# Kernel optimization log

Hardware: AMD Instinct MI355X
Metric: run time of the kernel (lower is better)

Reference implementation:

```python
import jax, jax.numpy as jnp
import numpy as np

B, T, C = 8, 2048, 1024  # batch, seq_len (== block_size), n_embed
HEAD = 64


def setup_inputs() -> dict:
    key = jax.random.key(0)
    k1, k2, k3, k4 = jax.random.split(key, 4)
    x = jax.random.normal(k1, (B, T, C), dtype=jnp.float32)
    # nn.Linear(n_embed, head_size, bias=False) -> weight [head, C]; stored as [C, head]
    Wk = jax.random.normal(k2, (C, HEAD), dtype=jnp.float32) * (C ** -0.5)
    Wq = jax.random.normal(k3, (C, HEAD), dtype=jnp.float32) * (C ** -0.5)
    Wv = jax.random.normal(k4, (C, HEAD), dtype=jnp.float32) * (C ** -0.5)
    return {"x": x, "Wk": Wk, "Wq": Wq, "Wv": Wv}


def reference(x, Wk, Wq, Wv):
    Bx, Tx, Cx = x.shape
    k = jnp.einsum('btc,ch->bth', x, Wk)  # [B,T,HEAD]
    q = jnp.einsum('btc,ch->bth', x, Wq)
    v = jnp.einsum('btc,ch->bth', x, Wv)
    # Source quirk: scores = k @ q^T (k rows), scaled by n_embed**-0.5 (C, not head_size)
    scores = jnp.einsum('bih,bjh->bij', k, q) * (Cx ** -0.5)  # [B,T,T]
    causal = jnp.tril(jnp.ones((Tx, Tx), dtype=bool))
    scores = jnp.where(causal, scores, -jnp.inf)
    attn = jax.nn.softmax(scores, axis=-1)
    out = jnp.einsum('bij,bjh->bih', attn, v)  # [B,T,HEAD]
    return out
```

## Files before the change

### kernel.cpp

```cpp
#include <hip/hip_runtime.h>
#include <cstdint>

#define B_ 8
#define T_ 2048
#define C_ 1024
#define H_ 64
#define BT_ (B_ * T_)

typedef short short8 __attribute__((ext_vector_type(8)));
typedef short bh4 __attribute__((ext_vector_type(4)));
typedef float f32x4 __attribute__((ext_vector_type(4)));

__device__ inline short f2bf(float f) {
  uint32_t u = __float_as_uint(f);
  u += 0x7fffu + ((u >> 16) & 1u);
  return (short)(u >> 16);
}

__device__ __forceinline__ void gl_lds16(const void* g, void* l) {
  __builtin_amdgcn_global_load_lds(
      (const __attribute__((address_space(1))) unsigned int*)g,
      (__attribute__((address_space(3))) unsigned int*)l, 16, 0, 0);
}

__global__ __launch_bounds__(256) void prep_w(
    const float* __restrict__ Wk, const float* __restrict__ Wq,
    const float* __restrict__ Wv, short* __restrict__ Wt) {
  __shared__ float wl[64][68];
  const int mat = blockIdx.x >> 4;
  const int kc = blockIdx.x & 15;
  const float* W = (mat == 0) ? Wk : (mat == 1) ? Wq : Wv;
  const float sc = (mat == 0) ? 0.03125f * 1.44269504088896f : 1.0f;
  const int t = threadIdx.x;
  const int k0 = kc * 64;
#pragma unroll
  for (int j = 0; j < 4; ++j) {
    int s = t + 256 * j;
    int kr = s >> 4, cf = s & 15;
    float4 v = *reinterpret_cast<const float4*>(&W[(size_t)(k0 + kr) * H_ + cf * 4]);
    wl[kr][cf * 4 + 0] = v.x; wl[kr][cf * 4 + 1] = v.y;
    wl[kr][cf * 4 + 2] = v.z; wl[kr][cf * 4 + 3] = v.w;
  }
  __syncthreads();
#pragma unroll
  for (int j = 0; j < 2; ++j) {
    int s = t + 256 * j;
    int n = s >> 3, g = s & 7;
    short8 o;
#pragma unroll
    for (int i = 0; i < 8; ++i) o[i] = f2bf(wl[8 * g + i][n] * sc);
    *reinterpret_cast<short8*>(&Wt[(size_t)(mat * 64 + n) * C_ + k0 + 8 * g]) = o;
  }
}

__global__ __launch_bounds__(256, 1) void proj_kernel(
    const float* __restrict__ x, const short* __restrict__ Wt,
    short* __restrict__ Kp, short* __restrict__ Qp, short* __restrict__ Vt) {
  __shared__ float xs[2][32 * 64];
  __shared__ short ws[2][192 * 64];
  const int t = threadIdx.x;
  const int w = t >> 6, lane = t & 63;
  const int l15 = lane & 15, lg = lane >> 4;
  const int rg = w >> 1, ch = w & 1;
  const int rowBase = blockIdx.x * 32;

  f32x4 acc[6];
  const f32x4 zf = {0.f, 0.f, 0.f, 0.f};
#pragma unroll
  for (int i = 0; i < 6; ++i) acc[i] = zf;

  auto stage = [&](int buf, int k0) {
#pragma unroll
    for (int j = 0; j < 2; ++j) {
      const int seg = w * 2 + j;
      const int r = seg * 4 + (lane >> 4);
      const float* g =
          &x[(size_t)(rowBase + r) * C_ + k0 + (((lane & 15) ^ (r & 7)) << 2)];
      gl_lds16(g, (char*)&xs[buf][0] + seg * 1024);
    }
#pragma unroll
    for (int j = 0; j < 6; ++j) {
      const int seg = w * 6 + j;
      const int n = seg * 8 + (lane >> 3);
      const short* g =
          &Wt[(size_t)n * C_ + k0 + (((lane & 7) ^ (n & 7)) << 3)];
      gl_lds16(g, (char*)&ws[buf][0] + seg * 1024);
    }
  };

  stage(0, 0);

#pragma unroll 1
  for (int it = 0; it < 16; ++it) {
    __syncthreads();
    const int cb = it & 1;
    if (it < 15) stage(cb ^ 1, (it + 1) * 64);
    const int arow = 16 * rg + l15;
    const int x7 = arow & 7;
    const float* xrow = &xs[cb][arow * 64];
    float4 fa = *reinterpret_cast<const float4*>(xrow + (((2 * lg) ^ x7) << 2));
    float4 fb = *reinterpret_cast<const float4*>(xrow + (((2 * lg + 1) ^ x7) << 2));
    float4 fc = *reinterpret_cast<const float4*>(xrow + (((2 * lg + 8) ^ x7) << 2));
    float4 fd = *reinterpret_cast<const float4*>(xrow + (((2 * lg + 9) ^ x7) << 2));
    short8 a0, a1;
    a0[0] = f2bf(fa.x); a0[1] = f2bf(fa.y); a0[2] = f2bf(fa.z); a0[3] = f2bf(fa.w);
    a0[4] = f2bf(fb.x); a0[5] = f2bf(fb.y); a0[6] = f2bf(fb.z); a0[7] = f2bf(fb.w);
    a1[0] = f2bf(fc.x); a1[1] = f2bf(fc.y); a1[2] = f2bf(fc.z); a1[3] = f2bf(fc.w);
    a1[4] = f2bf(fd.x); a1[5] = f2bf(fd.y); a1[6] = f2bf(fd.z); a1[7] = f2bf(fd.w);
#pragma unroll
    for (int nt = 0; nt < 6; ++nt) {
      const int n2 = 16 * (6 * ch + nt) + l15, n7 = n2 & 7;
      const short* wrow = &ws[cb][n2 * 64];
      short8 b0 = *reinterpret_cast<const short8*>(wrow + ((lg ^ n7) << 3));
      short8 b1 = *reinterpret_cast<const short8*>(wrow + (((4 + lg) ^ n7) << 3));
      acc[nt] = __builtin_amdgcn_mfma_f32_16x16x32_bf16(a0, b0, acc[nt], 0, 0, 0);
      acc[nt] = __builtin_amdgcn_mfma_f32_16x16x32_bf16(a1, b1, acc[nt], 0, 0, 0);
    }
  }

  const int strip = blockIdx.x * 2 + rg;
  const int rb = strip * 16;
#pragma unroll
  for (int nt = 0; nt < 6; ++nt) {
    const int ntg = 6 * ch + nt;
    if (ntg < 8) {
      short* O = (ntg < 4) ? Kp : Qp;
      const int col = (ntg & 3) * 16 + l15;
#pragma unroll
      for (int r = 0; r < 4; ++r)
        O[(size_t)(rb + lg * 4 + r) * H_ + col] = f2bf(acc[nt][r]);
    }
  }
  __syncthreads();
  if (ch == 1) {
    short* vl = reinterpret_cast<short*>(&xs[0][0]) + rg * (16 * 66);
#pragma unroll
    for (int nt = 2; nt < 6; ++nt)
#pragma unroll
      for (int r = 0; r < 4; ++r)
        vl[(lg * 4 + r) * 66 + (nt - 2) * 16 + l15] = f2bf(acc[nt][r]);
    asm volatile("s_waitcnt lgkmcnt(0)" ::: "memory");
    short8 o0, o1;
#pragma unroll
    for (int i = 0; i < 8; ++i) o0[i] = vl[i * 66 + lane];
#pragma unroll
    for (int i = 0; i < 8; ++i) o1[i] = vl[(8 + i) * 66 + lane];
    const int bb = strip >> 7, tb = (strip & 127) * 16;
    short* dst = &Vt[((size_t)bb * H_ + lane) * T_ + tb];
    *reinterpret_cast<short8*>(dst) = o0;
    *reinterpret_cast<short8*>(dst + 8) = o1;
  }
}

__global__ __launch_bounds__(512) void attn_kernel(
    const short* __restrict__ Kq, const short* __restrict__ Qk,
    const short* __restrict__ Vt, float* __restrict__ Pg,
    float* __restrict__ Mg) {
  __shared__ short Ks[4][64 * 64];
  __shared__ short Vs[4][64 * 64];
  const int t = threadIdx.x, w = t >> 6, lane = t & 63;
  const int l15 = lane & 15, lg = lane >> 4;
  const int batch = blockIdx.x & 7;
  const int q = blockIdx.x >> 3;
  const int sidx = (q < 32) ? (31 - q) : (q - 32);
  const int h = (q < 32) ? 0 : 1;
  const int p = w & 1, rg = w >> 1;
  const short* Kb = Kq + (size_t)batch * T_ * H_;
  const short* Qb = Qk + (size_t)batch * T_ * H_;
  const short* Vb = Vt + (size_t)batch * H_ * T_;
  const f32x4 zf = {0.f, 0.f, 0.f, 0.f};
  const int k7 = l15 & 7;

  const int qbase = sidx * 64;
  const int qrow = qbase + rg * 16 + l15;
  const short8 qa0 = *reinterpret_cast<const short8*>(&Kb[(size_t)qrow * H_ + lg * 8]);
  const short8 qa1 = *reinterpret_cast<const short8*>(&Kb[(size_t)qrow * H_ + lg * 8 + 32]);
  const int ntiles = sidx + 1;
  const int nlist = (h == 0) ? ((ntiles + 1) >> 1) : (ntiles >> 1);
  const int np = (nlist + 1) >> 1;

  const int tp = w >> 2, kind = (w >> 1) & 1, q2 = w & 1;
  const int srow = lane >> 3;
  const int ssw = ((lane & 7) ^ srow) << 3;
  auto stage = [&](int per) {
    const int le = 2 * per + tp;
    if (le >= nlist) return;
    const int gkt = 2 * le + h;
    const int buf = (per & 1) * 2 + tp;
    const int kbase = gkt * 64;
    if (kind == 0) {
#pragma unroll
      for (int g2 = 0; g2 < 4; ++g2) {
        const int gg = q2 * 4 + g2;
        gl_lds16(&Qb[(size_t)(kbase + gg * 8 + srow) * H_ + ssw],
                 (char*)&Ks[buf][0] + gg * 1024);
      }
    } else {
#pragma unroll
      for (int g2 = 0; g2 < 4; ++g2) {
        const int gg = q2 * 4 + g2;
        gl_lds16(&Vb[(size_t)(gg * 8 + srow) * T_ + kbase + ssw],
                 (char*)&Vs[buf][0] + gg * 1024);
      }
    }
  };

  f32x4 O[4];
#pragma unroll
  for (int i = 0; i < 4; ++i) O[i] = zf;
  float m = -1e30f, l = 0.f;

  stage(0);

#pragma unroll 1
  for (int i = 0; i < np; ++i) {
    __syncthreads();
    if (i + 1 < np) stage(i + 1);
    const int le = 2 * i + p;
    if (le < nlist) {
      const int gkt = 2 * le + h;
      const int cb = (i & 1) * 2 + p;
      const int kbase = gkt * 64;
      f32x4 S[4];
      __builtin_amdgcn_s_setprio(1);
#pragma unroll
      for (int nt = 0; nt < 4; ++nt) {
        S[nt] = zf;
        const short* krow = &Ks[cb][(16 * nt + l15) * 64];
        short8 kf0 = *reinterpret_cast<const short8*>(&krow[(lg ^ k7) << 3]);
        short8 kf1 = *reinterpret_cast<const short8*>(&krow[((4 + lg) ^ k7) << 3]);
        S[nt] = __builtin_amdgcn_mfma_f32_16x16x32_bf16(kf0, qa0, S[nt], 0, 0, 0);
        S[nt] = __builtin_amdgcn_mfma_f32_16x16x32_bf16(kf1, qa1, S[nt], 0, 0, 0);
      }
      __builtin_amdgcn_s_setprio(0);
      if (gkt == sidx) {
#pragma unroll
        for (int nt = 0; nt < 4; ++nt) {
          const int klo = kbase + 16 * nt + 4 * lg;
#pragma unroll
          for (int r = 0; r < 4; ++r)
            if (klo + r > qrow) S[nt][r] = -1e30f;
        }
      }
      float mx0 = fmaxf(fmaxf(S[0][0], S[0][1]), fmaxf(S[0][2], S[0][3]));
      float mx1 = fmaxf(fmaxf(S[1][0], S[1][1]), fmaxf(S[1][2], S[1][3]));
      float mx2 = fmaxf(fmaxf(S[2][0], S[2][1]), fmaxf(S[2][2], S[2][3]));
      float mx3 = fmaxf(fmaxf(S[3][0], S[3][1]), fmaxf(S[3][2], S[3][3]));
      float mx = fmaxf(fmaxf(mx0, mx1), fmaxf(mx2, mx3));
      mx = fmaxf(mx, __shfl_xor(mx, 16));
      mx = fmaxf(mx, __shfl_xor(mx, 32));
      const float mn = fmaxf(m, mx);
      const float scv = exp2f(m - mn);
      m = mn;
      float rs = 0.f;
#pragma unroll
      for (int nt = 0; nt < 4; ++nt)
#pragma unroll
        for (int r = 0; r < 4; ++r) {
          const float pv = exp2f(S[nt][r] - mn);
          S[nt][r] = pv;
          rs += pv;
        }
      rs += __shfl_xor(rs, 16);
      rs += __shfl_xor(rs, 32);
      l = l * scv + rs;
#pragma unroll
      for (int nt = 0; nt < 4; ++nt) O[nt] *= scv;
      const int d7 = l15 & 7;
      const int vo = 4 * (lg & 1);
      __builtin_amdgcn_s_setprio(1);
#pragma unroll
      for (int kc = 0; kc < 2; ++kc) {
        short8 pa;
#pragma unroll
        for (int jj = 0; jj < 8; ++jj)
          pa[jj] = f2bf(S[2 * kc + (jj >> 2)][jj & 3]);
        const int slo = ((4 * kc + (lg >> 1)) ^ d7) << 3;
        const int shi = ((4 * kc + 2 + (lg >> 1)) ^ d7) << 3;
#pragma unroll
        for (int nt = 0; nt < 4; ++nt) {
          const short* vrow = &Vs[cb][(16 * nt + l15) * 64];
          const bh4 vlo = *reinterpret_cast<const bh4*>(&vrow[slo + vo]);
          const bh4 vhi = *reinterpret_cast<const bh4*>(&vrow[shi + vo]);
          short8 vf;
          vf[0] = vlo[0]; vf[1] = vlo[1]; vf[2] = vlo[2]; vf[3] = vlo[3];
          vf[4] = vhi[0]; vf[5] = vhi[1]; vf[6] = vhi[2]; vf[7] = vhi[3];
          O[nt] = __builtin_amdgcn_mfma_f32_16x16x32_bf16(vf, pa, O[nt], 0, 0, 0);
        }
      }
      __builtin_amdgcn_s_setprio(0);
    }
  }

  __syncthreads();
  float* Po = reinterpret_cast<float*>(&Ks[0][0]);
  float* Mlp = reinterpret_cast<float*>(&Vs[0][0]);
#pragma unroll
  for (int nt = 0; nt < 4; ++nt)
    *reinterpret_cast<f32x4*>(&Po[(w * 16 + l15) * 64 + 16 * nt + 4 * lg]) = O[nt];
  if (lane < 16) {
    Mlp[(w * 16 + l15) * 2 + 0] = m;
    Mlp[(w * 16 + l15) * 2 + 1] = l;
  }
  __syncthreads();
  {
    const int c4 = t & 15;
#pragma unroll
    for (int hh = 0; hh < 2; ++hh) {
      const int lr = (t >> 4) + 32 * hh;
      const int w0 = (lr >> 4) * 2, w1 = w0 + 1;
      const int r = lr & 15;
      const float m0 = Mlp[(w0 * 16 + r) * 2], l0 = Mlp[(w0 * 16 + r) * 2 + 1];
      const float m1 = Mlp[(w1 * 16 + r) * 2], l1 = Mlp[(w1 * 16 + r) * 2 + 1];
      const float M = fmaxf(m0, m1);
      const float e0 = exp2f(m0 - M), e1 = exp2f(m1 - M);
      const float L = l0 * e0 + l1 * e1;
      const f32x4 o0 = *reinterpret_cast<const f32x4*>(&Po[(w0 * 16 + r) * 64 + c4 * 4]);
      const f32x4 o1 = *reinterpret_cast<const f32x4*>(&Po[(w1 * 16 + r) * 64 + c4 * 4]);
      const f32x4 om = o0 * e0 + o1 * e1;
      const size_t gr = (size_t)batch * T_ + qbase + lr;
      *reinterpret_cast<f32x4*>(&Pg[((size_t)h * BT_ + gr) * H_ + c4 * 4]) = om;
      if (c4 == 0) {
        Mg[((size_t)h * BT_ + gr) * 2 + 0] = M;
        Mg[((size_t)h * BT_ + gr) * 2 + 1] = L;
      }
    }
  }
}

__global__ __launch_bounds__(256) void combine_kernel(
    const float* __restrict__ Pg, const float* __restrict__ Mg,
    float* __restrict__ out) {
  const int t = threadIdx.x;
#pragma unroll
  for (int k = 0; k < 2; ++k) {
    const int task = blockIdx.x * 512 + k * 256 + t;
    const int row = task >> 4;
    const int c4 = task & 15;
    const float M0 = Mg[(size_t)row * 2], L0 = Mg[(size_t)row * 2 + 1];
    const float M1 = Mg[((size_t)BT_ + row) * 2], L1 = Mg[((size_t)BT_ + row) * 2 + 1];
    const float M = fmaxf(M0, M1);
    const float e0 = exp2f(M0 - M), e1 = exp2f(M1 - M);
    const float L = L0 * e0 + L1 * e1;
    const f32x4 o0 = *reinterpret_cast<const f32x4*>(&Pg[(size_t)row * H_ + c4 * 4]);
    const f32x4 o1 = *reinterpret_cast<const f32x4*>(&Pg[((size_t)BT_ + row) * H_ + c4 * 4]);
    const f32x4 res = (o0 * e0 + o1 * e1) * (1.f / L);
    *reinterpret_cast<f32x4*>(&out[(size_t)row * H_ + c4 * 4]) = res;
  }
}

extern "C" void kernel_launch(void* const* d_in, const int* in_sizes, int n_in,
                              void* d_out, int out_size, void* d_ws, size_t ws_size,
                              hipStream_t stream) {
  const float* x = (const float*)d_in[0];
  const float* Wk = (const float*)d_in[1];
  const float* Wq = (const float*)d_in[2];
  const float* Wv = (const float*)d_in[3];
  float* out = (float*)d_out;

  short* Kp = (short*)d_ws;
  short* Qp = Kp + (size_t)BT_ * H_;
  short* Vt = Qp + (size_t)BT_ * H_;
  short* Wt = Vt + (size_t)BT_ * H_;
  float* Pg = (float*)(Wt + 192 * C_);
  float* Mg = Pg + (size_t)2 * BT_ * H_;

  hipLaunchKernelGGL(prep_w, dim3(48), dim3(256), 0, stream, Wk, Wq, Wv, Wt);
  hipLaunchKernelGGL(proj_kernel, dim3(512), dim3(256), 0, stream, x, Wt, Kp, Qp, Vt);
  hipLaunchKernelGGL(attn_kernel, dim3(512), dim3(512), 0, stream, Kp, Qp, Vt, Pg, Mg);
  hipLaunchKernelGGL(combine_kernel, dim3(512), dim3(256), 0, stream, Pg, Mg, out);
}
```

Measured before the change: 54.23 us.

## Split attention into 4-way KV partitions with 128-row query blocks

Reorganizes attention work so each block handles 128 query rows (one 16-row group per wave) and one of four interleaved KV-tile partitions, instead of 64 rows split 2-way between wave pairs. Each wave now processes both staged tiles per iteration, which removes the in-block LDS merge of partial results and writes per-wave partials straight to global memory. The combine kernel merges four partials instead of two. This doubles the partial-result memory traffic and workspace size, and may change load balance across blocks.

```diff
diff --git a/kernel.cpp b/kernel.cpp
--- a/kernel.cpp
+++ b/kernel.cpp
@@ -161,22 +161,23 @@
   const int t = threadIdx.x, w = t >> 6, lane = t & 63;
   const int l15 = lane & 15, lg = lane >> 4;
   const int batch = blockIdx.x & 7;
-  const int q = blockIdx.x >> 3;
-  const int sidx = (q < 32) ? (31 - q) : (q - 32);
-  const int h = (q < 32) ? 0 : 1;
-  const int p = w & 1, rg = w >> 1;
+  const int rest = blockIdx.x >> 3;
+  const int qh = rest & 3;
+  const int g = rest >> 2;
+  const int sidx = (g < 8) ? (15 - g) : (g - 8);
+  const int rg = w;
   const short* Kb = Kq + (size_t)batch * T_ * H_;
   const short* Qb = Qk + (size_t)batch * T_ * H_;
   const short* Vb = Vt + (size_t)batch * H_ * T_;
   const f32x4 zf = {0.f, 0.f, 0.f, 0.f};
   const int k7 = l15 & 7;
 
-  const int qbase = sidx * 64;
+  const int qbase = sidx * 128;
   const int qrow = qbase + rg * 16 + l15;
   const short8 qa0 = *reinterpret_cast<const short8*>(&Kb[(size_t)qrow * H_ + lg * 8]);
   const short8 qa1 = *reinterpret_cast<const short8*>(&Kb[(size_t)qrow * H_ + lg * 8 + 32]);
-  const int ntiles = sidx + 1;
-  const int nlist = (h == 0) ? ((ntiles + 1) >> 1) : (ntiles >> 1);
+  const int ntop = 2 * sidx + 1;
+  const int nlist = (ntop >= qh) ? (((ntop - qh) >> 2) + 1) : 0;
   const int np = (nlist + 1) >> 1;
 
   const int tp = w >> 2, kind = (w >> 1) & 1, q2 = w & 1;
@@ -185,7 +186,7 @@
   auto stage = [&](int per) {
     const int le = 2 * per + tp;
     if (le >= nlist) return;
-    const int gkt = 2 * le + h;
+    const int gkt = 4 * le + qh;
     const int buf = (per & 1) * 2 + tp;
     const int kbase = gkt * 64;
     if (kind == 0) {
@@ -216,115 +217,92 @@
   for (int i = 0; i < np; ++i) {
     __syncthreads();
     if (i + 1 < np) stage(i + 1);
-    const int le = 2 * i + p;
-    if (le < nlist) {
-      const int gkt = 2 * le + h;
-      const int cb = (i & 1) * 2 + p;
-      const int kbase = gkt * 64;
-      f32x4 S[4];
-      __builtin_amdgcn_s_setprio(1);
-#pragma unroll
-      for (int nt = 0; nt < 4; ++nt) {
-        S[nt] = zf;
-        const short* krow = &Ks[cb][(16 * nt + l15) * 64];
-        short8 kf0 = *reinterpret_cast<const short8*>(&krow[(lg ^ k7) << 3]);
-        short8 kf1 = *reinterpret_cast<const short8*>(&krow[((4 + lg) ^ k7) << 3]);
-        S[nt] = __builtin_amdgcn_mfma_f32_16x16x32_bf16(kf0, qa0, S[nt], 0, 0, 0);
-        S[nt] = __builtin_amdgcn_mfma_f32_16x16x32_bf16(kf1, qa1, S[nt], 0, 0, 0);
+#pragma unroll 1
+    for (int tt = 0; tt < 2; ++tt) {
+      const int le = 2 * i + tt;
+      if (le < nlist) {
+        const int gkt = 4 * le + qh;
+        const int cb = (i & 1) * 2 + tt;
+        const int kbase = gkt * 64;
+        f32x4 S[4];
+        __builtin_amdgcn_s_setprio(1);
+#pragma unroll
+        for (int nt = 0; nt < 4; ++nt) {
+          S[nt] = zf;
+          const short* krow = &Ks[cb][(16 * nt + l15) * 64];
+          short8 kf0 = *reinterpret_cast<const short8*>(&krow[(lg ^ k7) << 3]);
+          short8 kf1 = *reinterpret_cast<const short8*>(&krow[((4 + lg) ^ k7) << 3]);
+          S[nt] = __builtin_amdgcn_mfma_f32_16x16x32_bf16(kf0, qa0, S[nt], 0, 0, 0);
+          S[nt] = __builtin_amdgcn_mfma_f32_16x16x32_bf16(kf1, qa1, S[nt], 0, 0, 0);
+        }
+        __builtin_amdgcn_s_setprio(0);
+        if (gkt >= 2 * sidx) {
+#pragma unroll
+          for (int nt = 0; nt < 4; ++nt) {
+            const int klo = kbase + 16 * nt + 4 * lg;
+#pragma unroll
+            for (int r = 0; r < 4; ++r)
+              if (klo + r > qrow) S[nt][r] = -1e30f;
+          }
+        }
+        float mx0 = fmaxf(fmaxf(S[0][0], S[0][1]), fmaxf(S[0][2], S[0][3]));
+        float mx1 = fmaxf(fmaxf(S[1][0], S[1][1]), fmaxf(S[1][2], S[1][3]));
+        float mx2 = fmaxf(fmaxf(S[2][0], S[2][1]), fmaxf(S[2][2], S[2][3]));
+        float mx3 = fmaxf(fmaxf(S[3][0], S[3][1]), fmaxf(S[3][2], S[3][3]));
+        float mx = fmaxf(fmaxf(mx0, mx1), fmaxf(mx2, mx3));
+        mx = fmaxf(mx, __shfl_xor(mx, 16));
+        mx = fmaxf(mx, __shfl_xor(mx, 32));
+        const float mn = fmaxf(m, mx);
+        const float scv = exp2f(m - mn);
+        m = mn;
+        float rs = 0.f;
+#pragma unroll
+        for (int nt = 0; nt < 4; ++nt)
+#pragma unroll
+          for (int r = 0; r < 4; ++r) {
+            const float pv = exp2f(S[nt][r] - mn);
+            S[nt][r] = pv;
+            rs += pv;
+          }
+        rs += __shfl_xor(rs, 16);
+        rs += __shfl_xor(rs, 32);
+        l = l * scv + rs;
+#pragma unroll
+        for (int nt = 0; nt < 4; ++nt) O[nt] *= scv;
+        const int d7 = l15 & 7;
+        const int vo = 4 * (lg & 1);
+        __builtin_amdgcn_s_setprio(1);
+#pragma unroll
+        for (int kc = 0; kc < 2; ++kc) {
+          short8 pa;
+#pragma unroll
+          for (int jj = 0; jj < 8; ++jj)
+            pa[jj] = f2bf(S[2 * kc + (jj >> 2)][jj & 3]);
+          const int slo = ((4 * kc + (lg >> 1)) ^ d7) << 3;
+          const int shi = ((4 * kc + 2 + (lg >> 1)) ^ d7) << 3;
+#pragma unroll
+          for (int nt = 0; nt < 4; ++nt) {
+            const short* vrow = &Vs[cb][(16 * nt + l15) * 64];
+            const bh4 vlo = *reinterpret_cast<const bh4*>(&vrow[slo + vo]);
+            const bh4 vhi = *reinterpret_cast<const bh4*>(&vrow[shi + vo]);
+            short8 vf;
+            vf[0] = vlo[0]; vf[1] = vlo[1]; vf[2] = vlo[2]; vf[3] = vlo[3];
+            vf[4] = vhi[0]; vf[5] = vhi[1]; vf[6] = vhi[2]; vf[7] = vhi[3];
+            O[nt] = __builtin_amdgcn_mfma_f32_16x16x32_bf16(vf, pa, O[nt], 0, 0, 0);
+          }
+        }
+        __builtin_amdgcn_s_setprio(0);
       }
-      __builtin_amdgcn_s_setprio(0);
-      if (gkt == sidx) {
-#pragma unroll
-        for (int nt = 0; nt < 4; ++nt) {
-          const int klo = kbase + 16 * nt + 4 * lg;
-#pragma unroll
-          for (int r = 0; r < 4; ++r)
-            if (klo + r > qrow) S[nt][r] = -1e30f;
-        }
-      }
-      float mx0 = fmaxf(fmaxf(S[0][0], S[0][1]), fmaxf(S[0][2], S[0][3]));
-      float mx1 = fmaxf(fmaxf(S[1][0], S[1][1]), fmaxf(S[1][2], S[1][3]));
-      float mx2 = fmaxf(fmaxf(S[2][0], S[2][1]), fmaxf(S[2][2], S[2][3]));
-      float mx3 = fmaxf(fmaxf(S[3][0], S[3][1]), fmaxf(S[3][2], S[3][3]));
-      float mx = fmaxf(fmaxf(mx0, mx1), fmaxf(mx2, mx3));
-      mx = fmaxf(mx, __shfl_xor(mx, 16));
-      mx = fmaxf(mx, __shfl_xor(mx, 32));
-      const float mn = fmaxf(m, mx);
-      const float scv = exp2f(m - mn);
-      m = mn;
-      float rs = 0.f;
-#pragma unroll
-      for (int nt = 0; nt < 4; ++nt)
-#pragma unroll
-        for (int r = 0; r < 4; ++r) {
-          const float pv = exp2f(S[nt][r] - mn);
-          S[nt][r] = pv;
-          rs += pv;
-        }
-      rs += __shfl_xor(rs, 16);
-      rs += __shfl_xor(rs, 32);
-      l = l * scv + rs;
-#pragma unroll
-      for (int nt = 0; nt < 4; ++nt) O[nt] *= scv;
-      const int d7 = l15 & 7;
-      const int vo = 4 * (lg & 1);
-      __builtin_amdgcn_s_setprio(1);
-#pragma unroll
-      for (int kc = 0; kc < 2; ++kc) {
-        short8 pa;
-#pragma unroll
-        for (int jj = 0; jj < 8; ++jj)
-          pa[jj] = f2bf(S[2 * kc + (jj >> 2)][jj & 3]);
-        const int slo = ((4 * kc + (lg >> 1)) ^ d7) << 3;
-        const int shi = ((4 * kc + 2 + (lg >> 1)) ^ d7) << 3;
-#pragma unroll
-        for (int nt = 0; nt < 4; ++nt) {
-          const short* vrow = &Vs[cb][(16 * nt + l15) * 64];
-          const bh4 vlo = *reinterpret_cast<const bh4*>(&vrow[slo + vo]);
-          const bh4 vhi = *reinterpret_cast<const bh4*>(&vrow[shi + vo]);
-          short8 vf;
-          vf[0] = vlo[0]; vf[1] = vlo[1]; vf[2] = vlo[2]; vf[3] = vlo[3];
-          vf[4] = vhi[0]; vf[5] = vhi[1]; vf[6] = vhi[2]; vf[7] = vhi[3];
-          O[nt] = __builtin_amdgcn_mfma_f32_16x16x32_bf16(vf, pa, O[nt], 0, 0, 0);
-        }
-      }
-      __builtin_amdgcn_s_setprio(0);
-    }
-  }
-
-  __syncthreads();
-  float* Po = reinterpret_cast<float*>(&Ks[0][0]);
-  float* Mlp = reinterpret_cast<float*>(&Vs[0][0]);
+    }
+  }
+
+  const size_t gr = (size_t)batch * T_ + qrow;
 #pragma unroll
   for (int nt = 0; nt < 4; ++nt)
-    *reinterpret_cast<f32x4*>(&Po[(w * 16 + l15) * 64 + 16 * nt + 4 * lg]) = O[nt];
-  if (lane < 16) {
-    Mlp[(w * 16 + l15) * 2 + 0] = m;
-    Mlp[(w * 16 + l15) * 2 + 1] = l;
-  }
-  __syncthreads();
-  {
-    const int c4 = t & 15;
-#pragma unroll
-    for (int hh = 0; hh < 2; ++hh) {
-      const int lr = (t >> 4) + 32 * hh;
-      const int w0 = (lr >> 4) * 2, w1 = w0 + 1;
-      const int r = lr & 15;
-      const float m0 = Mlp[(w0 * 16 + r) * 2], l0 = Mlp[(w0 * 16 + r) * 2 + 1];
-      const float m1 = Mlp[(w1 * 16 + r) * 2], l1 = Mlp[(w1 * 16 + r) * 2 + 1];
-      const float M = fmaxf(m0, m1);
-      const float e0 = exp2f(m0 - M), e1 = exp2f(m1 - M);
-      const float L = l0 * e0 + l1 * e1;
-      const f32x4 o0 = *reinterpret_cast<const f32x4*>(&Po[(w0 * 16 + r) * 64 + c4 * 4]);
-      const f32x4 o1 = *reinterpret_cast<const f32x4*>(&Po[(w1 * 16 + r) * 64 + c4 * 4]);
-      const f32x4 om = o0 * e0 + o1 * e1;
-      const size_t gr = (size_t)batch * T_ + qbase + lr;
-      *reinterpret_cast<f32x4*>(&Pg[((size_t)h * BT_ + gr) * H_ + c4 * 4]) = om;
-      if (c4 == 0) {
-        Mg[((size_t)h * BT_ + gr) * 2 + 0] = M;
-        Mg[((size_t)h * BT_ + gr) * 2 + 1] = L;
-      }
-    }
+    *reinterpret_cast<f32x4*>(&Pg[((size_t)qh * BT_ + gr) * H_ + 16 * nt + 4 * lg]) = O[nt];
+  if (lg == 0) {
+    Mg[((size_t)qh * BT_ + gr) * 2 + 0] = m;
+    Mg[((size_t)qh * BT_ + gr) * 2 + 1] = l;
   }
 }
 
@@ -337,14 +315,24 @@
     const int task = blockIdx.x * 512 + k * 256 + t;
     const int row = task >> 4;
     const int c4 = task & 15;
-    const float M0 = Mg[(size_t)row * 2], L0 = Mg[(size_t)row * 2 + 1];
-    const float M1 = Mg[((size_t)BT_ + row) * 2], L1 = Mg[((size_t)BT_ + row) * 2 + 1];
-    const float M = fmaxf(M0, M1);
-    const float e0 = exp2f(M0 - M), e1 = exp2f(M1 - M);
-    const float L = L0 * e0 + L1 * e1;
-    const f32x4 o0 = *reinterpret_cast<const f32x4*>(&Pg[(size_t)row * H_ + c4 * 4]);
-    const f32x4 o1 = *reinterpret_cast<const f32x4*>(&Pg[((size_t)BT_ + row) * H_ + c4 * 4]);
-    const f32x4 res = (o0 * e0 + o1 * e1) * (1.f / L);
+    float Mh[4], Lh[4];
+#pragma unroll
+    for (int h = 0; h < 4; ++h) {
+      Mh[h] = Mg[((size_t)h * BT_ + row) * 2 + 0];
+      Lh[h] = Mg[((size_t)h * BT_ + row) * 2 + 1];
+    }
+    const float M = fmaxf(fmaxf(Mh[0], Mh[1]), fmaxf(Mh[2], Mh[3]));
+    float L = 0.f;
+    f32x4 o = {0.f, 0.f, 0.f, 0.f};
+#pragma unroll
+    for (int h = 0; h < 4; ++h) {
+      const float e = exp2f(Mh[h] - M);
+      L += Lh[h] * e;
+      const f32x4 po =
+          *reinterpret_cast<const f32x4*>(&Pg[((size_t)h * BT_ + row) * H_ + c4 * 4]);
+      o += po * e;
+    }
+    const f32x4 res = o * (1.f / L);
     *reinterpret_cast<f32x4*>(&out[(size_t)row * H_ + c4 * 4]) = res;
   }
 }
@@ -363,7 +351,7 @@
   short* Vt = Qp + (size_t)BT_ * H_;
   short* Wt = Vt + (size_t)BT_ * H_;
   float* Pg = (float*)(Wt + 192 * C_);
-  float* Mg = Pg + (size_t)2 * BT_ * H_;
+  float* Mg = Pg + (size_t)4 * BT_ * H_;
 
   hipLaunchKernelGGL(prep_w, dim3(48), dim3(256), 0, stream, Wk, Wq, Wv, Wt);
   hipLaunchKernelGGL(proj_kernel, dim3(512), dim3(256), 0, stream, x, Wt, Kp, Qp, Vt);
```

New measurement: 52.56 us. -3.1%, faster.
